# Kernel tuning notes

Hardware: AMD Instinct MI355X
Metric: run time of the kernel (lower is better)

Reference implementation:

```python
import jax, jax.numpy as jnp
import numpy as np

EPS = 1e-5

def _layernorm(x, g, b):
    mu = jnp.mean(x, axis=-1, keepdims=True)
    var = jnp.mean((x - mu) ** 2, axis=-1, keepdims=True)
    return (x - mu) * jax.lax.rsqrt(var + EPS) * g + b

def setup_inputs() -> dict:
    key = jax.random.key(0)
    ks = jax.random.split(key, 16)
    B, C, H, W = 2, 64, 96, 96
    HID = 256
    s = 0.02
    inp = {
        "x": jax.random.normal(ks[0], (B, C, H, W), dtype=jnp.float32),
        "mask": jax.random.randint(ks[1], (B, H, W), 0, 2, dtype=jnp.int32),
        "wq": jax.random.normal(ks[2], (C, C), dtype=jnp.float32) * s,
        "bq": jnp.zeros((C,), dtype=jnp.float32),
        "wk": jax.random.normal(ks[3], (C, C), dtype=jnp.float32) * s,
        "bk": jnp.zeros((C,), dtype=jnp.float32),
        "wv": jax.random.normal(ks[4], (C, C), dtype=jnp.float32) * s,
        "bv": jnp.zeros((C,), dtype=jnp.float32),
        "wo": jax.random.normal(ks[5], (C, C), dtype=jnp.float32) * s,
        "bo": jnp.zeros((C,), dtype=jnp.float32),
        "g1": jnp.ones((C,), dtype=jnp.float32),
        "b1": jnp.zeros((C,), dtype=jnp.float32),
        "g2": jnp.ones((C,), dtype=jnp.float32),
        "b2": jnp.zeros((C,), dtype=jnp.float32),
        "w1": jax.random.normal(ks[6], (HID, C), dtype=jnp.float32) * s,
        "bf1": jnp.zeros((HID,), dtype=jnp.float32),
        "w2": jax.random.normal(ks[7], (C, HID), dtype=jnp.float32) * s,
        "bf2": jnp.zeros((C,), dtype=jnp.float32),
    }
    return inp

def reference(x, mask, wq, bq, wk, bk, wv, bv, wo, bo, g1, b1, g2, b2, w1, bf1, w2, bf2):
    B, C, H, W = x.shape
    scale = C ** (-0.5)
    xf = jnp.transpose(x, (0, 2, 3, 1)).reshape(B, H * W, C)   # [B,N,C]
    m = mask.reshape(B, H * W).astype(bool)                     # [B,N] valid pillars
    # pre-norm (original norms the gathered valid feats; LN is per-token so dense is equivalent)
    h = _layernorm(xf, g1, b1)
    q = h @ wq.T + bq
    k = h @ wk.T + bk
    v = h @ wv.T + bv
    scores = jnp.einsum('bnc,bmc->bnm', q, k) * scale
    scores = jnp.where(m[:, None, :], scores, -1e9)            # attend only among valid keys
    attn = jax.nn.softmax(scores, axis=-1)
    att = jnp.einsum('bnm,bmc->bnc', attn, v)
    h2 = h + (att @ wo.T + bo)                                  # residual onto norm1 output (as in source)
    h2 = _layernorm(h2, g2, b2)
    out = h2 + (jax.nn.gelu(h2 @ w1.T + bf1, approximate=False) @ w2.T + bf2)
    out = jnp.where(m[:, :, None], out, 0.0)                    # scatter-back: invalid positions are zeros
    return jnp.transpose(out.reshape(B, H, W, C), (0, 3, 1, 2))
```

## Files before the change

kernel.cpp:

```cpp
#include <hip/hip_runtime.h>

#define HW     9216
#define NTOK   18432
#define SPLITS 8
#define KIT    (HW / SPLITS / 32)

typedef float  floatx4 __attribute__((ext_vector_type(4)));
typedef short  short8  __attribute__((ext_vector_type(8)));
typedef short  short4v __attribute__((ext_vector_type(4)));
typedef int    int4v   __attribute__((ext_vector_type(4)));

#if __has_builtin(__builtin_amdgcn_exp2f)
#define EXP2F(x) __builtin_amdgcn_exp2f(x)
#else
#define EXP2F(x) exp2f(x)
#endif

__device__ __forceinline__ unsigned short f2bf(float f) {
  unsigned int u = __float_as_uint(f);
  u += 0x7fffu + ((u >> 16) & 1u);
  return (unsigned short)(u >> 16);
}
__device__ __forceinline__ float bf2f(unsigned short s) {
  return __uint_as_float(((unsigned int)s) << 16);
}
__device__ __forceinline__ int pk2(float a, float b) {
  unsigned ua = __float_as_uint(a) + 0x8000u;
  unsigned ub = __float_as_uint(b) + 0x8000u;
  return (int)((ua >> 16) | (ub & 0xffff0000u));
}

__global__ __launch_bounds__(256) void k_qkv(
    const float* __restrict__ x,
    const float* __restrict__ wq, const float* __restrict__ bq,
    const float* __restrict__ wk, const float* __restrict__ bk,
    const float* __restrict__ wv, const float* __restrict__ bv,
    const float* __restrict__ g1, const float* __restrict__ b1,
    const int* __restrict__ mask,
    const float* __restrict__ wo, const float* __restrict__ w1,
    const float* __restrict__ w2,
    unsigned short* __restrict__ h_bf, unsigned short* __restrict__ qg,
    unsigned short* __restrict__ ksw, unsigned short* __restrict__ vsw,
    float* __restrict__ maskf, unsigned short* __restrict__ wobf,
    unsigned short* __restrict__ w1bf, unsigned short* __restrict__ w2bf,
    float* __restrict__ cntb)
{
  __shared__ float xt[64][33];
  __shared__ float hb[32][64];
  __shared__ unsigned short kt[32][72];
  __shared__ unsigned short vt[64][40];

  const int tid = threadIdx.x, wid = tid >> 6, c = tid & 63;
  const int bx = blockIdx.x;
  const int t0 = bx * 32;
  const int b  = t0 / HW, n0 = t0 % HW;

  if (tid < 32) maskf[t0 + tid] = mask[t0 + tid] ? 1.f : 0.f;
  if (wid == 0) {
    const bool mm = (c < 32) ? (mask[t0 + c] == 0) : false;
    const unsigned long long bal = __ballot(mm);
    if (c == 0) cntb[bx] = (float)__popcll(bal);
  }
  if (bx < 16)       { const int i = bx * 256 + tid;        wobf[i] = f2bf(wo[i]); }
  else if (bx < 80)  { const int i = (bx - 16) * 256 + tid; w1bf[i] = f2bf(w1[i]); }
  else if (bx < 144) { const int i = (bx - 80) * 256 + tid; w2bf[i] = f2bf(w2[i]); }

  #pragma unroll
  for (int p = 0; p < 2; ++p) {
    const int idx = p * 256 + tid;
    const int cc = idx >> 3, t4 = (idx & 7) * 4;
    const floatx4 v = *(const floatx4*)(x + ((long)b * 64 + cc) * HW + n0 + t4);
    xt[cc][t4 + 0] = v[0]; xt[cc][t4 + 1] = v[1];
    xt[cc][t4 + 2] = v[2]; xt[cc][t4 + 3] = v[3];
  }
  __syncthreads();

  const float g1v = g1[c], b1v = b1[c];
  float aq[8], ak[8], av[8];
  const float bqv = bq[c], bkv = bk[c], bvv = bv[c];

  #pragma unroll
  for (int tt = 0; tt < 8; ++tt) {
    const int tok = wid * 8 + tt;
    const float val = xt[c][tok];
    float s = val, q = val * val;
    #pragma unroll
    for (int d = 1; d < 64; d <<= 1) { s += __shfl_xor(s, d); q += __shfl_xor(q, d); }
    const float mu  = s * (1.f / 64.f);
    const float var = q * (1.f / 64.f) - mu * mu;
    const float hv  = (val - mu) * rsqrtf(var + 1e-5f) * g1v + b1v;
    hb[tok][c] = hv;
    h_bf[(long)(t0 + tok) * 64 + c] = f2bf(hv);
    aq[tt] = bqv; ak[tt] = bkv; av[tt] = bvv;
  }

  const floatx4* wq4 = (const floatx4*)(wq + c * 64);
  const floatx4* wk4 = (const floatx4*)(wk + c * 64);
  const floatx4* wv4 = (const floatx4*)(wv + c * 64);
  #pragma unroll
  for (int i = 0; i < 16; ++i) {
    const floatx4 wqv = wq4[i], wkv = wk4[i], wvv = wv4[i];
    #pragma unroll
    for (int tt = 0; tt < 8; ++tt) {
      const floatx4 hh = *(const floatx4*)&hb[wid * 8 + tt][i * 4];
      aq[tt] = fmaf(wqv[0],hh[0], fmaf(wqv[1],hh[1], fmaf(wqv[2],hh[2], fmaf(wqv[3],hh[3], aq[tt]))));
      ak[tt] = fmaf(wkv[0],hh[0], fmaf(wkv[1],hh[1], fmaf(wkv[2],hh[2], fmaf(wkv[3],hh[3], ak[tt]))));
      av[tt] = fmaf(wvv[0],hh[0], fmaf(wvv[1],hh[1], fmaf(wvv[2],hh[2], fmaf(wvv[3],hh[3], av[tt]))));
    }
  }

  const float QSC = 0.125f * 1.44269504088896f;
  #pragma unroll
  for (int tt = 0; tt < 8; ++tt) {
    const int tok = wid * 8 + tt;
    const float mk = mask[t0 + tok] ? 1.f : 0.f;
    qg[(long)(t0 + tok) * 64 + c] = f2bf(aq[tt] * QSC);
    kt[tok][c] = f2bf(ak[tt] * mk);
    vt[c][tok] = f2bf(av[tt] * mk);
  }
  __syncthreads();

  const long tile = (long)b * 288 + (n0 >> 5);
  {
    const int slot = tid >> 6, l = tid & 63;
    const int m = l & 15, qd = l >> 4, sub = slot >> 1, ss = slot & 1;
    const short8 v8 = *(const short8*)(&kt[sub * 16 + m][ss * 32 + qd * 8]);
    *(short8*)(ksw + tile * 2048 + tid * 8) = v8;
  }
  {
    const int f = tid >> 6, l = tid & 63;
    const int m = l & 15, qd = l >> 4;
    const short4v lo = *(const short4v*)(&vt[f * 16 + m][qd * 4]);
    const short4v hi = *(const short4v*)(&vt[f * 16 + m][16 + qd * 4]);
    short8 v8;
    v8[0] = lo[0]; v8[1] = lo[1]; v8[2] = lo[2]; v8[3] = lo[3];
    v8[4] = hi[0]; v8[5] = hi[1]; v8[6] = hi[2]; v8[7] = hi[3];
    *(short8*)(vsw + tile * 2048 + tid * 8) = v8;
  }
}

__global__ __launch_bounds__(256, 4) void k_attn(
    const unsigned short* __restrict__ qg, const unsigned short* __restrict__ ksw,
    const unsigned short* __restrict__ vsw,
    unsigned short* __restrict__ opart, float* __restrict__ lpart)
{
  __shared__ __align__(16) char smem[17408];

  const int tid = threadIdx.x, wid = tid >> 6, lane = tid & 63;
  const int mcol = lane & 15, quad = lane >> 4;
  const int bx = blockIdx.x;
  const int split = bx & (SPLITS - 1), qidx = bx / SPLITS;
  const int b = qidx / 48, qt = qidx % 48;
  const long t0q = (long)b * HW + qt * 192 + wid * 48;

  const unsigned short* kswt = ksw + ((long)b * 288 + split * KIT) * 2048;
  const unsigned short* vswt = vsw + ((long)b * 288 + split * KIT) * 2048;

  short8 qf[3][2];
  #pragma unroll
  for (int g = 0; g < 3; ++g)
    #pragma unroll
    for (int s = 0; s < 2; ++s)
      qf[g][s] = *(const short8*)(qg + (t0q + g * 16 + mcol) * 64 + s * 32 + quad * 8);

  short8 ones8;
  #pragma unroll
  for (int i = 0; i < 8; ++i) ones8[i] = (short)0x3F80;

  floatx4 oT[3][4], oL[3];
  #pragma unroll
  for (int g = 0; g < 3; ++g) {
    #pragma unroll
    for (int f = 0; f < 4; ++f) oT[g][f] = (floatx4){0.f,0.f,0.f,0.f};
    oL[g] = (floatx4){0.f,0.f,0.f,0.f};
  }

  short8 kr = *(const short8*)(kswt + tid * 8);
  short8 vr = *(const short8*)(vswt + tid * 8);
  *(short8*)((unsigned short*)smem + tid * 8) = kr;
  *(short8*)((unsigned short*)(smem + 4096) + tid * 8) = vr;
  __syncthreads();

  for (int it = 0; it < KIT; ++it) {
    const int off = (it & 1) * 8192;
    const unsigned short* kfc = (const unsigned short*)(smem + off);
    const unsigned short* vfc = (const unsigned short*)(smem + off + 4096);
    if (it + 1 < KIT) {
      kr = *(const short8*)(kswt + (it + 1) * 2048 + tid * 8);
      vr = *(const short8*)(vswt + (it + 1) * 2048 + tid * 8);
    }

    const short8 kA00 = *(const short8*)(kfc + (0 * 64 + lane) * 8);
    const short8 kA01 = *(const short8*)(kfc + (1 * 64 + lane) * 8);
    const short8 kA10 = *(const short8*)(kfc + (2 * 64 + lane) * 8);
    const short8 kA11 = *(const short8*)(kfc + (3 * 64 + lane) * 8);

    short8 pf[3];
    #pragma unroll
    for (int g = 0; g < 3; ++g) {
      floatx4 s0 = (floatx4){0.f,0.f,0.f,0.f}, s1 = (floatx4){0.f,0.f,0.f,0.f};
      s0 = __builtin_amdgcn_mfma_f32_16x16x32_bf16(kA00, qf[g][0], s0, 0, 0, 0);
      s0 = __builtin_amdgcn_mfma_f32_16x16x32_bf16(kA01, qf[g][1], s0, 0, 0, 0);
      s1 = __builtin_amdgcn_mfma_f32_16x16x32_bf16(kA10, qf[g][0], s1, 0, 0, 0);
      s1 = __builtin_amdgcn_mfma_f32_16x16x32_bf16(kA11, qf[g][1], s1, 0, 0, 0);

      int4v pv;
      pv[0] = pk2(EXP2F(s0[0]), EXP2F(s0[1]));
      pv[1] = pk2(EXP2F(s0[2]), EXP2F(s0[3]));
      pv[2] = pk2(EXP2F(s1[0]), EXP2F(s1[1]));
      pv[3] = pk2(EXP2F(s1[2]), EXP2F(s1[3]));
      pf[g] = __builtin_bit_cast(short8, pv);
      oL[g] = __builtin_amdgcn_mfma_f32_16x16x32_bf16(ones8, pf[g], oL[g], 0, 0, 0);
    }

    #pragma unroll
    for (int f = 0; f < 4; ++f) {
      const short8 vA = *(const short8*)(vfc + (f * 64 + lane) * 8);
      #pragma unroll
      for (int g = 0; g < 3; ++g)
        oT[g][f] = __builtin_amdgcn_mfma_f32_16x16x32_bf16(vA, pf[g], oT[g][f], 0, 0, 0);
    }

    if (it + 1 < KIT) {
      unsigned short* kfn = (unsigned short*)(smem + (off ^ 8192));
      unsigned short* vfn = (unsigned short*)(smem + (off ^ 8192) + 4096);
      *(short8*)(kfn + tid * 8) = kr;
      *(short8*)(vfn + tid * 8) = vr;
    }
    __syncthreads();
  }

  float* scr = (float*)smem + wid * 1088;
  #pragma unroll
  for (int g = 0; g < 3; ++g) {
    #pragma unroll
    for (int f = 0; f < 4; ++f)
      #pragma unroll
      for (int r = 0; r < 4; ++r)
        scr[(quad * 4 + r) * 68 + f * 16 + mcol] = oT[g][f][r];
    #pragma unroll
    for (int ps = 0; ps < 2; ++ps) {
      const int row = ps * 8 + (lane >> 3), cb = (lane & 7) * 8;
      const floatx4 a = *(const floatx4*)(scr + row * 68 + cb);
      const floatx4 c = *(const floatx4*)(scr + row * 68 + cb + 4);
      int4v pk;
      pk[0] = pk2(a[0], a[1]); pk[1] = pk2(a[2], a[3]);
      pk[2] = pk2(c[0], c[1]); pk[3] = pk2(c[2], c[3]);
      *(int4v*)(opart + ((long)split * NTOK + t0q + g * 16 + row) * 64 + cb) = pk;
    }
  }
  if (lane < 16) {
    #pragma unroll
    for (int g = 0; g < 3; ++g)
      lpart[(long)split * NTOK + t0q + g * 16 + lane] = oL[g][0];
  }
}

__global__ __launch_bounds__(256) void k_post(
    const unsigned short* __restrict__ opart, const float* __restrict__ lpart,
    const unsigned short* __restrict__ h_bf, const float* __restrict__ maskf,
    const float* __restrict__ cntb,
    const unsigned short* __restrict__ wobf, const float* __restrict__ bo,
    const float* __restrict__ g2, const float* __restrict__ b2,
    const unsigned short* __restrict__ w1bf, const float* __restrict__ bf1,
    const unsigned short* __restrict__ w2bf, const float* __restrict__ bf2,
    float* __restrict__ out)
{
  __shared__ float          h2_lds[32 * 68];
  __shared__ unsigned short att_lds[32 * 72];
  __shared__ unsigned short hn_lds[32 * 72];
  __shared__ unsigned short g_lds[32 * 264];
  __shared__ float          ot_lds[32 * 68];
  __shared__ float          linv[32];
  __shared__ float          st_mu[32], st_rs[32];
  __shared__ float          nred[4];

  const int tid = threadIdx.x, wid = tid >> 6, lane = tid & 63;
  const int mcol = lane & 15, quad = lane >> 4;
  const int t0 = blockIdx.x * 32;
  const int b = t0 / HW, n0 = t0 % HW;

  {
    float cacc = 0.f;
    for (int i = tid; i < 288; i += 256) cacc += cntb[b * 288 + i];
    #pragma unroll
    for (int d = 1; d < 64; d <<= 1) cacc += __shfl_xor(cacc, d);
    if (lane == 0) nred[wid] = cacc;
  }

  const int tok = tid >> 3, c8 = (tid & 7) * 8;
  float o[8];
  #pragma unroll
  for (int i = 0; i < 8; ++i) o[i] = 0.f;
  #pragma unroll
  for (int s = 0; s < SPLITS; ++s) {
    const short8 op = *(const short8*)(opart + ((long)s * NTOK + t0 + tok) * 64 + c8);
    #pragma unroll
    for (int i = 0; i < 8; ++i) o[i] += bf2f((unsigned short)op[i]);
  }
  const short8 hb8 = *(const short8*)(h_bf + (long)(t0 + tok) * 64 + c8);
  const floatx4 bo0 = *(const floatx4*)(bo + c8);
  const floatx4 bo1 = *(const floatx4*)(bo + c8 + 4);
  __syncthreads();

  if (tid < 32) {
    float l = -((nred[0] + nred[1]) + (nred[2] + nred[3]));
    #pragma unroll
    for (int s = 0; s < SPLITS; ++s) l += lpart[(long)s * NTOK + t0 + tid];
    linv[tid] = 1.0f / l;
  }
  __syncthreads();
  {
    const float sc = linv[tok];
    int4v av;
    av[0] = pk2(o[0]*sc, o[1]*sc); av[1] = pk2(o[2]*sc, o[3]*sc);
    av[2] = pk2(o[4]*sc, o[5]*sc); av[3] = pk2(o[6]*sc, o[7]*sc);
    *(int4v*)(att_lds + tok * 72 + c8) = av;
    floatx4 h20, h21;
    #pragma unroll
    for (int i = 0; i < 4; ++i) {
      h20[i] = bf2f((unsigned short)hb8[i])     + bo0[i];
      h21[i] = bf2f((unsigned short)hb8[i + 4]) + bo1[i];
    }
    *(floatx4*)(h2_lds + tok * 68 + c8)     = h20;
    *(floatx4*)(h2_lds + tok * 68 + c8 + 4) = h21;
  }
  __syncthreads();

  const int Mt = wid & 1, nbase = (wid >> 1) * 2;
  {
    const short8 aA0 = *(const short8*)(att_lds + (Mt * 16 + mcol) * 72 + quad * 8);
    const short8 aA1 = *(const short8*)(att_lds + (Mt * 16 + mcol) * 72 + 32 + quad * 8);
    #pragma unroll
    for (int nt = 0; nt < 2; ++nt) {
      const int nc = (nbase + nt) * 16;
      const short8 b0 = *(const short8*)(wobf + (nc + mcol) * 64 + quad * 8);
      const short8 b1 = *(const short8*)(wobf + (nc + mcol) * 64 + 32 + quad * 8);
      floatx4 d = (floatx4){0.f,0.f,0.f,0.f};
      d = __builtin_amdgcn_mfma_f32_16x16x32_bf16(aA0, b0, d, 0, 0, 0);
      d = __builtin_amdgcn_mfma_f32_16x16x32_bf16(aA1, b1, d, 0, 0, 0);
      #pragma unroll
      for (int r = 0; r < 4; ++r)
        h2_lds[(Mt * 16 + quad * 4 + r) * 68 + nc + mcol] += d[r];
    }
  }
  __syncthreads();

  {
    floatx4 v0 = *(const floatx4*)(h2_lds + tok * 68 + c8);
    floatx4 v1 = *(const floatx4*)(h2_lds + tok * 68 + c8 + 4);
    float s1 = (v0[0]+v0[1])+(v0[2]+v0[3]) + (v1[0]+v1[1])+(v1[2]+v1[3]);
    float s2 = (v0[0]*v0[0]+v0[1]*v0[1])+(v0[2]*v0[2]+v0[3]*v0[3])
             + (v1[0]*v1[0]+v1[1]*v1[1])+(v1[2]*v1[2]+v1[3]*v1[3]);
    #pragma unroll
    for (int d = 1; d < 8; d <<= 1) { s1 += __shfl_xor(s1, d); s2 += __shfl_xor(s2, d); }
    if ((tid & 7) == 0) {
      const float mu = s1 * (1.f / 64.f);
      const float var = s2 * (1.f / 64.f) - mu * mu;
      st_mu[tok] = mu; st_rs[tok] = rsqrtf(var + 1e-5f);
    }
  }
  __syncthreads();

  {
    const float mu = st_mu[tok], rs = st_rs[tok];
    const floatx4 v0 = *(const floatx4*)(h2_lds + tok * 68 + c8);
    const floatx4 v1 = *(const floatx4*)(h2_lds + tok * 68 + c8 + 4);
    const floatx4 ga = *(const floatx4*)(g2 + c8), gb = *(const floatx4*)(g2 + c8 + 4);
    const floatx4 ba = *(const floatx4*)(b2 + c8), bb = *(const floatx4*)(b2 + c8 + 4);
    float hn[8];
    #pragma unroll
    for (int i = 0; i < 4; ++i) {
      hn[i]     = (v0[i] - mu) * rs * ga[i] + ba[i];
      hn[i + 4] = (v1[i] - mu) * rs * gb[i] + bb[i];
    }
    int4v hv;
    hv[0] = pk2(hn[0], hn[1]); hv[1] = pk2(hn[2], hn[3]);
    hv[2] = pk2(hn[4], hn[5]); hv[3] = pk2(hn[6], hn[7]);
    *(int4v*)(hn_lds + tok * 72 + c8) = hv;
  }
  __syncthreads();

  {
    const short8 aA0 = *(const short8*)(hn_lds + (Mt * 16 + mcol) * 72 + quad * 8);
    const short8 aA1 = *(const short8*)(hn_lds + (Mt * 16 + mcol) * 72 + 32 + quad * 8);
    #pragma unroll
    for (int nt = 0; nt < 8; ++nt) {
      const int u0 = ((wid >> 1) * 8 + nt) * 16;
      const short8 b0 = *(const short8*)(w1bf + (u0 + mcol) * 64 + quad * 8);
      const short8 b1 = *(const short8*)(w1bf + (u0 + mcol) * 64 + 32 + quad * 8);
      floatx4 d = (floatx4){0.f,0.f,0.f,0.f};
      d = __builtin_amdgcn_mfma_f32_16x16x32_bf16(aA0, b0, d, 0, 0, 0);
      d = __builtin_amdgcn_mfma_f32_16x16x32_bf16(aA1, b1, d, 0, 0, 0);
      const float bf1v = bf1[u0 + mcol];
      #pragma unroll
      for (int r = 0; r < 4; ++r) {
        const float a = d[r] + bf1v;
        const float gl = 0.5f * a * (1.0f + erff(a * 0.70710678118654752f));
        g_lds[(Mt * 16 + quad * 4 + r) * 264 + u0 + mcol] = f2bf(gl);
      }
    }
  }
  __syncthreads();

  {
    floatx4 acc[2];
    acc[0] = (floatx4){0.f,0.f,0.f,0.f}; acc[1] = (floatx4){0.f,0.f,0.f,0.f};
    #pragma unroll
    for (int ks = 0; ks < 8; ++ks) {
      const short8 aA = *(const short8*)(g_lds + (Mt * 16 + mcol) * 264 + ks * 32 + quad * 8);
      #pragma unroll
      for (int nt = 0; nt < 2; ++nt) {
        const int nc = (nbase + nt) * 16;
        const short8 bB = *(const short8*)(w2bf + (nc + mcol) * 256 + ks * 32 + quad * 8);
        acc[nt] = __builtin_amdgcn_mfma_f32_16x16x32_bf16(aA, bB, acc[nt], 0, 0, 0);
      }
    }
    #pragma unroll
    for (int nt = 0; nt < 2; ++nt) {
      const int cc = (nbase + nt) * 16 + mcol;
      const float g2v = g2[cc], b2v = b2[cc], bf2v = bf2[cc];
      #pragma unroll
      for (int r = 0; r < 4; ++r) {
        const int tokr = Mt * 16 + quad * 4 + r;
        const float hn = (h2_lds[tokr * 68 + cc] - st_mu[tokr]) * st_rs[tokr] * g2v + b2v;
        const float o2 = (hn + acc[nt][r] + bf2v) * maskf[t0 + tokr];
        ot_lds[tokr * 68 + cc] = o2;
      }
    }
  }
  __syncthreads();

  {
    const int c = tid >> 2, tg = (tid & 3) * 8;
    floatx4 v0, v1;
    #pragma unroll
    for (int i = 0; i < 4; ++i) {
      v0[i] = ot_lds[(tg + i) * 68 + c];
      v1[i] = ot_lds[(tg + 4 + i) * 68 + c];
    }
    float* dst = out + ((long)b * 64 + c) * HW + n0 + tg;
    *(floatx4*)dst = v0;
    *(floatx4*)(dst + 4) = v1;
  }
}

extern "C" void kernel_launch(void* const* d_in, const int* in_sizes, int n_in,
                              void* d_out, int out_size, void* d_ws, size_t ws_size,
                              hipStream_t stream) {
  (void)in_sizes; (void)n_in; (void)out_size; (void)ws_size;
  const float* x   = (const float*)d_in[0];
  const int*   msk = (const int*)  d_in[1];
  const float* wq  = (const float*)d_in[2];
  const float* bq  = (const float*)d_in[3];
  const float* wk  = (const float*)d_in[4];
  const float* bk  = (const float*)d_in[5];
  const float* wv  = (const float*)d_in[6];
  const float* bv  = (const float*)d_in[7];
  const float* wo  = (const float*)d_in[8];
  const float* bo  = (const float*)d_in[9];
  const float* g1  = (const float*)d_in[10];
  const float* b1  = (const float*)d_in[11];
  const float* g2  = (const float*)d_in[12];
  const float* b2  = (const float*)d_in[13];
  const float* w1  = (const float*)d_in[14];
  const float* bf1 = (const float*)d_in[15];
  const float* w2  = (const float*)d_in[16];
  const float* bf2 = (const float*)d_in[17];
  float* out = (float*)d_out;

  char* ws = (char*)d_ws;
  size_t off = 0;
  unsigned short* h_bf  = (unsigned short*)(ws + off); off += 2359296;
  unsigned short* qg    = (unsigned short*)(ws + off); off += 2359296;
  unsigned short* ksw   = (unsigned short*)(ws + off); off += 2359296;
  unsigned short* vsw   = (unsigned short*)(ws + off); off += 2359296;
  unsigned short* opart = (unsigned short*)(ws + off); off += (size_t)SPLITS * NTOK * 64 * 2;
  float*          lpart = (float*)(ws + off);          off += (size_t)SPLITS * NTOK * 4;
  float*          maskf = (float*)(ws + off);          off += 73728;
  unsigned short* wobf  = (unsigned short*)(ws + off); off += 8192;
  unsigned short* w1bf  = (unsigned short*)(ws + off); off += 32768;
  unsigned short* w2bf  = (unsigned short*)(ws + off); off += 32768;
  float*          cntb  = (float*)(ws + off);          off += 2304;

  k_qkv<<<dim3(576), dim3(256), 0, stream>>>(
      x, wq, bq, wk, bk, wv, bv, g1, b1, msk, wo, w1, w2,
      h_bf, qg, ksw, vsw, maskf, wobf, w1bf, w2bf, cntb);
  k_attn<<<dim3(96 * SPLITS), dim3(256), 0, stream>>>(qg, ksw, vsw, opart, lpart);
  k_post<<<dim3(576), dim3(256), 0, stream>>>(
      opart, lpart, h_bf, maskf, cntb, wobf, bo, g2, b2, w1bf, bf1, w2bf, bf2, out);
}
```

Before: 171.5 us.

## Compute QKV projection with bf16 MFMA and vectorize q/h stores

Replaces the scalar fp32 FMA QKV projection in k_qkv with bf16 MFMA 16x16x32 instructions. Each block converts wq/wk/wv to bf16 in a shared-memory buffer that aliases the x-transpose tile, and keeps the layernormed tokens in bf16 in shared memory. Q outputs are staged in shared memory so h and q can be written to global memory with 16-byte vector stores. In exchange, every block redoes the weight conversion, adds extra barriers, and the projection now uses bf16 inputs instead of fp32, which costs precision.

Result: faster. 160.7 us (-6.3%).

```diff
diff --git a/kernel.cpp b/kernel.cpp
--- a/kernel.cpp
+++ b/kernel.cpp
@@ -45,17 +45,27 @@
     unsigned short* __restrict__ w1bf, unsigned short* __restrict__ w2bf,
     float* __restrict__ cntb)
 {
-  __shared__ float xt[64][33];
-  __shared__ float hb[32][64];
+  __shared__ __align__(16) char usmem[27648];
+  float (*xt)[33] = (float (*)[33])usmem;
+  unsigned short (*wb)[64][72] = (unsigned short (*)[64][72])usmem;
+
+  __shared__ unsigned short hq[32][72];
   __shared__ unsigned short kt[32][72];
   __shared__ unsigned short vt[64][40];
+  __shared__ unsigned short qt[32][72];
+  __shared__ float mk32[32];
 
   const int tid = threadIdx.x, wid = tid >> 6, c = tid & 63;
+  const int mcol = c & 15, quad = c >> 4;
   const int bx = blockIdx.x;
   const int t0 = bx * 32;
   const int b  = t0 / HW, n0 = t0 % HW;
 
-  if (tid < 32) maskf[t0 + tid] = mask[t0 + tid] ? 1.f : 0.f;
+  if (tid < 32) {
+    const float m = mask[t0 + tid] ? 1.f : 0.f;
+    maskf[t0 + tid] = m;
+    mk32[tid] = m;
+  }
   if (wid == 0) {
     const bool mm = (c < 32) ? (mask[t0 + c] == 0) : false;
     const unsigned long long bal = __ballot(mm);
@@ -75,50 +85,91 @@
   }
   __syncthreads();
 
-  const float g1v = g1[c], b1v = b1[c];
-  float aq[8], ak[8], av[8];
-  const float bqv = bq[c], bkv = bk[c], bvv = bv[c];
-
-  #pragma unroll
-  for (int tt = 0; tt < 8; ++tt) {
-    const int tok = wid * 8 + tt;
-    const float val = xt[c][tok];
-    float s = val, q = val * val;
-    #pragma unroll
-    for (int d = 1; d < 64; d <<= 1) { s += __shfl_xor(s, d); q += __shfl_xor(q, d); }
-    const float mu  = s * (1.f / 64.f);
-    const float var = q * (1.f / 64.f) - mu * mu;
-    const float hv  = (val - mu) * rsqrtf(var + 1e-5f) * g1v + b1v;
-    hb[tok][c] = hv;
-    h_bf[(long)(t0 + tok) * 64 + c] = f2bf(hv);
-    aq[tt] = bqv; ak[tt] = bkv; av[tt] = bvv;
-  }
-
-  const floatx4* wq4 = (const floatx4*)(wq + c * 64);
-  const floatx4* wk4 = (const floatx4*)(wk + c * 64);
-  const floatx4* wv4 = (const floatx4*)(wv + c * 64);
-  #pragma unroll
-  for (int i = 0; i < 16; ++i) {
-    const floatx4 wqv = wq4[i], wkv = wk4[i], wvv = wv4[i];
+  {
+    const float g1v = g1[c], b1v = b1[c];
     #pragma unroll
     for (int tt = 0; tt < 8; ++tt) {
-      const floatx4 hh = *(const floatx4*)&hb[wid * 8 + tt][i * 4];
-      aq[tt] = fmaf(wqv[0],hh[0], fmaf(wqv[1],hh[1], fmaf(wqv[2],hh[2], fmaf(wqv[3],hh[3], aq[tt]))));
-      ak[tt] = fmaf(wkv[0],hh[0], fmaf(wkv[1],hh[1], fmaf(wkv[2],hh[2], fmaf(wkv[3],hh[3], ak[tt]))));
-      av[tt] = fmaf(wvv[0],hh[0], fmaf(wvv[1],hh[1], fmaf(wvv[2],hh[2], fmaf(wvv[3],hh[3], av[tt]))));
-    }
-  }
-
-  const float QSC = 0.125f * 1.44269504088896f;
-  #pragma unroll
-  for (int tt = 0; tt < 8; ++tt) {
-    const int tok = wid * 8 + tt;
-    const float mk = mask[t0 + tok] ? 1.f : 0.f;
-    qg[(long)(t0 + tok) * 64 + c] = f2bf(aq[tt] * QSC);
-    kt[tok][c] = f2bf(ak[tt] * mk);
-    vt[c][tok] = f2bf(av[tt] * mk);
-  }
-  __syncthreads();
+      const int tok = wid * 8 + tt;
+      const float val = xt[c][tok];
+      float s = val, q = val * val;
+      #pragma unroll
+      for (int d = 1; d < 64; d <<= 1) { s += __shfl_xor(s, d); q += __shfl_xor(q, d); }
+      const float mu  = s * (1.f / 64.f);
+      const float var = q * (1.f / 64.f) - mu * mu;
+      const float hv  = (val - mu) * rsqrtf(var + 1e-5f) * g1v + b1v;
+      hq[tok][c] = f2bf(hv);
+    }
+  }
+  __syncthreads();
+
+  {
+    const int tok = tid >> 3, c8 = (tid & 7) * 8;
+    *(short8*)(h_bf + (long)(t0 + tok) * 64 + c8) = *(const short8*)(&hq[tok][c8]);
+  }
+
+  {
+    auto conv = [&](const float* __restrict__ W, int mwi) {
+      #pragma unroll
+      for (int j = 0; j < 4; ++j) {
+        const int idx4 = (j * 256 + tid) * 4;
+        const int o = idx4 >> 6, in4 = idx4 & 63;
+        const floatx4 w4 = *(const floatx4*)(W + idx4);
+        short4v s4;
+        s4[0] = (short)f2bf(w4[0]); s4[1] = (short)f2bf(w4[1]);
+        s4[2] = (short)f2bf(w4[2]); s4[3] = (short)f2bf(w4[3]);
+        *(short4v*)(&wb[mwi][o][in4]) = s4;
+      }
+    };
+    conv(wq, 0); conv(wk, 1); conv(wv, 2);
+  }
+  __syncthreads();
+
+  {
+    const float QSC = 0.125f * 1.44269504088896f;
+    #pragma unroll
+    for (int i = 0; i < 6; ++i) {
+      const int t = wid * 6 + i;
+      const int mat  = t >> 3;
+      const int tokT = (t >> 2) & 1;
+      const int outT = t & 3;
+      const int out  = outT * 16 + mcol;
+      const short8 A0 = *(const short8*)(&hq[tokT * 16 + mcol][quad * 8]);
+      const short8 A1 = *(const short8*)(&hq[tokT * 16 + mcol][32 + quad * 8]);
+      const short8 B0 = *(const short8*)(&wb[mat][out][quad * 8]);
+      const short8 B1 = *(const short8*)(&wb[mat][out][32 + quad * 8]);
+      floatx4 d = (floatx4){0.f, 0.f, 0.f, 0.f};
+      d = __builtin_amdgcn_mfma_f32_16x16x32_bf16(A0, B0, d, 0, 0, 0);
+      d = __builtin_amdgcn_mfma_f32_16x16x32_bf16(A1, B1, d, 0, 0, 0);
+      if (mat == 0) {
+        const float bias = bq[out];
+        #pragma unroll
+        for (int r = 0; r < 4; ++r) {
+          const int tok = tokT * 16 + quad * 4 + r;
+          qt[tok][out] = f2bf((d[r] + bias) * QSC);
+        }
+      } else if (mat == 1) {
+        const float bias = bk[out];
+        #pragma unroll
+        for (int r = 0; r < 4; ++r) {
+          const int tok = tokT * 16 + quad * 4 + r;
+          kt[tok][out] = f2bf((d[r] + bias) * mk32[tok]);
+        }
+      } else {
+        const float bias = bv[out];
+        #pragma unroll
+        for (int r = 0; r < 4; ++r) {
+          const int tok = tokT * 16 + quad * 4 + r;
+          vt[out][tok] = f2bf((d[r] + bias) * mk32[tok]);
+        }
+      }
+    }
+  }
+  __syncthreads();
+
+  {
+    const int tok = tid >> 3, c8 = (tid & 7) * 8;
+    *(short8*)(qg + (long)(t0 + tok) * 64 + c8) = *(const short8*)(&qt[tok][c8]);
+  }
 
   const long tile = (long)b * 288 + (n0 >> 5);
   {
```
